# Performance work log

Measured on AMD Instinct MI355X. Metric: run time of the kernel, lower is better.

The kernel has to match this reference:

```python
import jax, jax.numpy as jnp
import numpy as np

B, S, HID, NH, CACHE = 2, 1024, 1024, 16, 4096
HD = HID // NH
HOT = max(4, CACHE // 4)
COLD = CACHE - HOT
COMP = HID // 2
EPS = 1e-5


def setup_inputs() -> dict:
    key = jax.random.key(0)
    ks = jax.random.split(key, 16)
    std = 0.02
    inp = {
        'inputs': jax.random.normal(ks[0], (B, S, HID), jnp.float32),
        'hot_keys': std * jax.random.normal(ks[1], (HOT, HID), jnp.float32),
        'hot_values': std * jax.random.normal(ks[2], (HOT, HID), jnp.float32),
        'hot_age': jnp.zeros((HOT,), jnp.float32),
        'hot_access': jnp.zeros((HOT,), jnp.float32),
        'cold_keys': std * jax.random.normal(ks[3], (COLD, HID), jnp.float32),
        'cold_values': std * jax.random.normal(ks[4], (COLD, HID), jnp.float32),
        'cold_age': jnp.zeros((COLD,), jnp.float32),
        'cold_access': jnp.zeros((COLD,), jnp.float32),
        # linear weights stored [in, out] (y = x @ W + b)
        'Wq': std * jax.random.normal(ks[5], (HID, HID), jnp.float32),
        'bq': jnp.zeros((HID,), jnp.float32),
        'Wk': std * jax.random.normal(ks[6], (HID, HID), jnp.float32),
        'bk': jnp.zeros((HID,), jnp.float32),
        'Wv': std * jax.random.normal(ks[7], (HID, HID), jnp.float32),
        'bv': jnp.zeros((HID,), jnp.float32),
        'Wo': std * jax.random.normal(ks[8], (HID, HID), jnp.float32),
        'bo': jnp.zeros((HID,), jnp.float32),
        'Wc': (1.0 / np.sqrt(HID)) * jax.random.normal(ks[9], (HID, COMP), jnp.float32),
        'bc': jnp.zeros((COMP,), jnp.float32),
        'Wd': (1.0 / np.sqrt(COMP)) * jax.random.normal(ks[10], (COMP, HID), jnp.float32),
        'bd': jnp.zeros((HID,), jnp.float32),
        'gamma': jnp.ones((HID,), jnp.float32),
        'beta': jnp.zeros((HID,), jnp.float32),
    }
    return inp


def _cache_level(q, cache_k, v_flat, age, access, Wk, bk, Wo, bo):
    # q: [B, NH, S, HD]; cache_k/v_flat: [C, HID]
    C = cache_k.shape[0]
    k = (cache_k @ Wk + bk).reshape(C, NH, HD)
    v = v_flat.reshape(C, NH, HD)
    scores = jnp.einsum('bhsd,chd->bhsc', q, k) / np.sqrt(HD)
    scores = scores + (-0.1 * age + 0.05 * access)  # broadcast over [B,H,S,C]
    attn = jax.nn.softmax(scores, axis=-1)
    out = jnp.einsum('bhsc,chd->bhsd', attn, v)
    out = out.transpose(0, 2, 1, 3).reshape(q.shape[0], q.shape[2], HID)
    return out @ Wo + bo


def reference(inputs, hot_keys, hot_values, hot_age, hot_access,
              cold_keys, cold_values, cold_age, cold_access,
              Wq, bq, Wk, bk, Wv, bv, Wo, bo, Wc, bc, Wd, bd, gamma, beta):
    q = (inputs @ Wq + bq).reshape(B, S, NH, HD).transpose(0, 2, 1, 3)
    # hot tier: values through value_net
    hot_v = hot_values @ Wv + bv
    hot_out = _cache_level(q, hot_keys, hot_v, hot_age, hot_access, Wk, bk, Wo, bo)
    # cold tier: values through compressor -> decompressor
    cold_v = (cold_values @ Wc + bc) @ Wd + bd
    cold_out = _cache_level(q, cold_keys, cold_v, cold_age, cold_access, Wk, bk, Wo, bo)
    x = hot_out + cold_out
    mu = jnp.mean(x, axis=-1, keepdims=True)
    var = jnp.mean(jnp.square(x - mu), axis=-1, keepdims=True)
    return (x - mu) / jnp.sqrt(var + EPS) * gamma + beta
```

## Files before the change

kernel.cpp:

```cpp
#include <hip/hip_runtime.h>

#define BBATCH 2
#define SS   1024
#define HID  1024
#define NH   16
#define HD   64
#define HOT  1024
#define COLD 3072
#define COMP 512

typedef __attribute__((ext_vector_type(8))) short s8v;
typedef __attribute__((ext_vector_type(4))) float f4v;
typedef unsigned short u16;
typedef unsigned int   u32;

__device__ __forceinline__ float b2f(u16 u){ return __uint_as_float(((u32)u)<<16); }
__device__ __forceinline__ u16 f2b(float f){
  u32 u = __float_as_uint(f);
  u += 0x7FFF + ((u>>16)&1);
  return (u16)(u>>16);
}
__device__ __forceinline__ u32 pk2r(u32 a, u32 b){
  return __builtin_amdgcn_perm(b + 0x8000u, a + 0x8000u, 0x07060302u);
}
__device__ __forceinline__ float ldsc(const void* p, int i, int isf32){
  return isf32 ? ((const float*)p)[i] : b2f(((const u16*)p)[i]);
}

__global__ void detect_kernel(const u32* __restrict__ gamma_raw, u32* __restrict__ flag){
  if (threadIdx.x == 0) flag[0] = (gamma_raw[0] == 0x3F800000u) ? 1u : 0u;
}

__global__ __launch_bounds__(256) void bias_kernel(
    const void* __restrict__ h_age, const void* __restrict__ h_acc,
    const void* __restrict__ c_age, const void* __restrict__ c_acc,
    float* __restrict__ BiasH, float* __restrict__ BiasC, const u32* __restrict__ flag)
{
  const int f = (int)flag[0];
  const int i = blockIdx.x * 256 + threadIdx.x;
  if (i < HOT) BiasH[i] = -0.1f * ldsc(h_age, i, f) + 0.05f * ldsc(h_acc, i, f);
  const int j = i - HOT;
  if (j >= 0 && j < COLD) BiasC[j] = -0.1f * ldsc(c_age, j, f) + 0.05f * ldsc(c_acc, j, f);
}

struct CDesc { const void* S; u16* D; int tile0, pad; };
struct CBatch { CDesc d[5]; int nd; };

__global__ __launch_bounds__(256) void convert_multi(CBatch cb, const u32* __restrict__ flag)
{
  int di = 0;
  for (int i = 1; i < cb.nd; i++) if ((int)blockIdx.x >= cb.d[i].tile0) di = i;
  const CDesc g = cb.d[di];
  const int f = (int)flag[0];
  const size_t e0 = (size_t)(blockIdx.x - g.tile0) * 2048 + (size_t)threadIdx.x * 8;
  if (f) {
    const float* s = (const float*)g.S + e0;
    const uint4 x = *(const uint4*)s, y = *(const uint4*)(s + 4);
    *(uint4*)(g.D + e0) =
      (uint4){ pk2r(x.x,x.y), pk2r(x.z,x.w), pk2r(y.x,y.y), pk2r(y.z,y.w) };
  } else {
    *(uint4*)(g.D + e0) = *(const uint4*)((const u16*)g.S + e0);
  }
}

struct TDesc { const void* S; u16* D; int R, C, cshift, tile0; };
struct TBatch { TDesc d[6]; int nd; };

__global__ __launch_bounds__(256) void transpose_kernel(TBatch tb, const u32* __restrict__ flag)
{
  __shared__ __align__(16) u16 Tt[64][72];
  int di = 0;
  for (int i = 1; i < tb.nd; i++) if ((int)blockIdx.x >= tb.d[i].tile0) di = i;
  const TDesc g = tb.d[di];
  const int local = blockIdx.x - g.tile0;
  const int ty = local >> g.cshift;
  const int tx = local & ((1 << g.cshift) - 1);
  const int r0 = ty * 64, c0 = tx * 64;
  const int f = (int)flag[0];
  const int t = threadIdx.x;
  const int sr = t >> 2, sc = (t & 3) * 16;

  union { uint4 q[2]; u16 h[16]; } u;
  if (f) {
    const float* s = (const float*)g.S + (size_t)(r0 + sr) * g.C + c0 + sc;
    const uint4 a = *(const uint4*)s,     b = *(const uint4*)(s + 4);
    const uint4 c = *(const uint4*)(s + 8), d2 = *(const uint4*)(s + 12);
    u.q[0] = (uint4){ pk2r(a.x,a.y), pk2r(a.z,a.w), pk2r(b.x,b.y), pk2r(b.z,b.w) };
    u.q[1] = (uint4){ pk2r(c.x,c.y), pk2r(c.z,c.w), pk2r(d2.x,d2.y), pk2r(d2.z,d2.w) };
  } else {
    const u16* s = (const u16*)g.S + (size_t)(r0 + sr) * g.C + c0 + sc;
    u.q[0] = *(const uint4*)s;  u.q[1] = *(const uint4*)(s + 8);
  }
  #pragma unroll
  for (int i = 0; i < 16; i++) Tt[sc + i][sr] = u.h[i];
  __syncthreads();

  const int dc = t >> 2, dr = (t & 3) * 16;
  const uint4 o0 = *(const uint4*)&Tt[dc][dr];
  const uint4 o1 = *(const uint4*)&Tt[dc][dr + 8];
  u16* dp = g.D + (size_t)(c0 + dc) * g.R + r0 + dr;
  *(uint4*)dp = o0;  *(uint4*)(dp + 8) = o1;
}

#define BM 128
#define BN 64
#define BK 32
struct GemmDesc {
  const void* A; const u16* BT; const void* bias; u16* C;
  int aflag, bcol0, M, N, K, nxlog, tile0, ctrans;
  float bias_scale;
};
struct GemmBatch { GemmDesc d[6]; int nd; };

__global__ __launch_bounds__(256) void gemm_multi(GemmBatch bat, const u32* __restrict__ flag)
{
  __shared__ __align__(16) u16 As[BM][BK + 8];
  __shared__ __align__(16) u16 Bs[BN][BK + 8];

  int di = 0;
  for (int i = 1; i < bat.nd; i++) if ((int)blockIdx.x >= bat.d[i].tile0) di = i;
  const GemmDesc g = bat.d[di];
  const int local = blockIdx.x - g.tile0;
  const int ty = local >> g.nxlog;
  const int tx = local - (ty << g.nxlog);
  const int m0 = ty * BM, n0 = tx * BN;

  const int f  = (int)flag[0];
  const int af = g.aflag ? f : 0;

  const int tid  = threadIdx.x;
  const int lane = tid & 63, wave = tid >> 6;
  const int quad = lane >> 4, l15 = lane & 15;
  const int wy = wave >> 1, wx = wave & 1;

  f4v acc[4][2];
  #pragma unroll
  for (int i = 0; i < 4; i++)
    #pragma unroll
    for (int j = 0; j < 2; j++) acc[i][j] = (f4v){0.f,0.f,0.f,0.f};

  const int ar = tid >> 1, ac = (tid & 1) * 16;
  const int br = tid >> 2, bc = (tid & 3) * 8;

  uint4 a0, a1, a2, a3;
  uint4 b0;

  auto load_tile = [&](int kk) {
    if (af) {
      const float* s = (const float*)g.A + (size_t)(m0 + ar) * g.K + kk + ac;
      a0 = *(const uint4*)s;       a1 = *(const uint4*)(s + 4);
      a2 = *(const uint4*)(s + 8); a3 = *(const uint4*)(s + 12);
    } else {
      const u16* s = (const u16*)g.A + (size_t)(m0 + ar) * g.K + kk + ac;
      a0 = *(const uint4*)s;  a1 = *(const uint4*)(s + 8);
    }
    const u16* bs = g.BT + (size_t)(g.bcol0 + n0 + br) * g.K + kk + bc;
    b0 = *(const uint4*)bs;
  };

  load_tile(0);

  for (int k0 = 0; k0 < g.K; k0 += BK) {
    __syncthreads();
    if (af) {
      *(uint4*)&As[ar][ac] =
        (uint4){ pk2r(a0.x,a0.y), pk2r(a0.z,a0.w), pk2r(a1.x,a1.y), pk2r(a1.z,a1.w) };
      *(uint4*)&As[ar][ac + 8] =
        (uint4){ pk2r(a2.x,a2.y), pk2r(a2.z,a2.w), pk2r(a3.x,a3.y), pk2r(a3.z,a3.w) };
    } else {
      *(uint4*)&As[ar][ac] = a0;  *(uint4*)&As[ar][ac + 8] = a1;
    }
    *(uint4*)&Bs[br][bc] = b0;
    __syncthreads();

    if (k0 + BK < g.K) load_tile(k0 + BK);

    s8v afr[4], bfr[2];
    #pragma unroll
    for (int i = 0; i < 4; i++)
      afr[i] = *(const s8v*)&As[wy * 64 + i * 16 + l15][quad * 8];
    #pragma unroll
    for (int j = 0; j < 2; j++)
      bfr[j] = *(const s8v*)&Bs[wx * 32 + j * 16 + l15][quad * 8];

    #pragma unroll
    for (int j = 0; j < 2; j++)
      #pragma unroll
      for (int i = 0; i < 4; i++)
        acc[i][j] = __builtin_amdgcn_mfma_f32_16x16x32_bf16(afr[i], bfr[j], acc[i][j], 0, 0, 0);
  }

  if (g.ctrans) {
    #pragma unroll
    for (int j = 0; j < 2; j++) {
      const int col = n0 + wx * 32 + j * 16 + l15;
      const float bv = ldsc(g.bias, g.bcol0 + col, f) * g.bias_scale;
      #pragma unroll
      for (int i = 0; i < 4; i++) {
        const int row = m0 + wy * 64 + i * 16 + quad * 4;
        u16 t4[4];
        #pragma unroll
        for (int r = 0; r < 4; r++) t4[r] = f2b(acc[i][j][r] + bv);
        *(uint2*)&g.C[(size_t)col * g.M + row] = *(uint2*)t4;
      }
    }
  } else {
    #pragma unroll
    for (int j = 0; j < 2; j++) {
      const int col = n0 + wx * 32 + j * 16 + l15;
      const float bv = ldsc(g.bias, g.bcol0 + col, f) * g.bias_scale;
      #pragma unroll
      for (int i = 0; i < 4; i++) {
        const int row = m0 + wy * 64 + i * 16 + quad * 4;
        #pragma unroll
        for (int r = 0; r < 4; r++)
          g.C[(size_t)(row + r) * g.N + col] = f2b(acc[i][j][r] + bv);
      }
    }
  }
}

#define KV(row, blk) (((row) << 6) + ((((blk) ^ ((row) & 7))) << 3))

__global__ __launch_bounds__(256, 4) void attn_kernel(
    const u16* __restrict__ Q,
    const u16* __restrict__ KHg, const u16* __restrict__ VHT,
    const u16* __restrict__ KCg, const u16* __restrict__ VCT,
    const float* __restrict__ BiasH, const float* __restrict__ BiasC,
    float* __restrict__ HotOut, float* __restrict__ ColdNum3, float* __restrict__ ColdZ3,
    int NG, int glog)
{
  __shared__ __align__(16) u16 Ks[64 * 64];
  __shared__ __align__(16) u16 Vs[64 * 64];

  const int tid  = threadIdx.x;
  const int lane = tid & 63, wave = tid >> 6;
  const int quad = lane >> 4, l15 = lane & 15;

  const int bx    = blockIdx.x;
  const int slice = bx & 3;
  const int sblk  = (bx >> 2) & 15;
  const int h     = (bx >> 6) & ((1 << glog) - 1);
  const int b     = bx >> (6 + glog);

  const int rowbase = b * SS + sblk * 64;
  const int hoff  = h * HD;
  const int myrow = wave * 16;

  const bool hot = (slice == 0);
  const u16*  Kt   = hot ? KHg : KCg;
  const u16*  Vt   = hot ? VHT : VCT;
  const float* Bias = hot ? BiasH : BiasC;
  const int   e0  = hot ? 0 : (slice - 1) * 1024;
  const int   ldv = hot ? HOT : COLD;

  const u16* qp = Q + (size_t)(rowbase + myrow + l15) * NG + hoff + quad * 8;
  const s8v aq0 = *(const s8v*)qp;
  const s8v aq1 = *(const s8v*)(qp + 32);

  const int rk = tid >> 2, cb2 = (tid & 3) * 2, sk = (tid & 3) * 16;
  const u16* kbase = Kt + (size_t)(e0 + rk) * NG + hoff + sk;
  const u16* vbase = Vt + (size_t)(hoff + rk) * ldv + e0 + sk;
  uint4 kr0 = *(const uint4*)kbase, kr1 = *(const uint4*)(kbase + 8);
  uint4 vr0 = *(const uint4*)vbase, vr1 = *(const uint4*)(vbase + 8);

  u16* kw0 = &Ks[KV(rk, cb2)];     u16* kw1 = &Ks[KV(rk, cb2 + 1)];
  u16* vw0 = &Vs[KV(rk, cb2)];     u16* vw1 = &Vs[KV(rk, cb2 + 1)];

  f4v o[4];
  #pragma unroll
  for (int j = 0; j < 4; j++) o[j] = (f4v){0.f,0.f,0.f,0.f};
  float zs = 0.f;

  for (int c0 = 0; c0 < 1024; c0 += 64) {
    __syncthreads();
    *(uint4*)kw0 = kr0;  *(uint4*)kw1 = kr1;
    *(uint4*)vw0 = vr0;  *(uint4*)vw1 = vr1;
    __syncthreads();
    if (c0 + 64 < 1024) {
      const u16* kn = kbase + (size_t)(c0 + 64) * NG;
      const u16* vn = vbase + (c0 + 64);
      kr0 = *(const uint4*)kn;  kr1 = *(const uint4*)(kn + 8);
      vr0 = *(const uint4*)vn;  vr1 = *(const uint4*)(vn + 8);
    }

    #pragma unroll
    for (int h2 = 0; h2 < 2; h2++) {
      const s8v ka0 = *(const s8v*)&Ks[KV(h2 * 32 + l15, quad)];
      const s8v ka1 = *(const s8v*)&Ks[KV(h2 * 32 + l15, 4 + quad)];
      const s8v kb0 = *(const s8v*)&Ks[KV(h2 * 32 + 16 + l15, quad)];
      const s8v kb1 = *(const s8v*)&Ks[KV(h2 * 32 + 16 + l15, 4 + quad)];
      f4v s0 = (f4v){0.f,0.f,0.f,0.f}, s1 = (f4v){0.f,0.f,0.f,0.f};
      s0 = __builtin_amdgcn_mfma_f32_16x16x32_bf16(ka0, aq0, s0, 0, 0, 0);
      s0 = __builtin_amdgcn_mfma_f32_16x16x32_bf16(ka1, aq1, s0, 0, 0, 0);
      s1 = __builtin_amdgcn_mfma_f32_16x16x32_bf16(kb0, aq0, s1, 0, 0, 0);
      s1 = __builtin_amdgcn_mfma_f32_16x16x32_bf16(kb1, aq1, s1, 0, 0, 0);

      const int cg0 = e0 + c0 + h2 * 32 + quad * 4;
      const float4 bi0 = *(const float4*)&Bias[cg0];
      const float4 bi1 = *(const float4*)&Bias[cg0 + 16];
      float p0[4], p1[4];
      p0[0] = __expf(fminf(s0[0] * 0.125f + bi0.x, 30.f));
      p0[1] = __expf(fminf(s0[1] * 0.125f + bi0.y, 30.f));
      p0[2] = __expf(fminf(s0[2] * 0.125f + bi0.z, 30.f));
      p0[3] = __expf(fminf(s0[3] * 0.125f + bi0.w, 30.f));
      p1[0] = __expf(fminf(s1[0] * 0.125f + bi1.x, 30.f));
      p1[1] = __expf(fminf(s1[1] * 0.125f + bi1.y, 30.f));
      p1[2] = __expf(fminf(s1[2] * 0.125f + bi1.z, 30.f));
      p1[3] = __expf(fminf(s1[3] * 0.125f + bi1.w, 30.f));
      zs += p0[0] + p0[1] + p0[2] + p0[3] + p1[0] + p1[1] + p1[2] + p1[3];

      const u32 W0 = pk2r(__float_as_uint(p0[0]), __float_as_uint(p0[1]));
      const u32 W1 = pk2r(__float_as_uint(p0[2]), __float_as_uint(p0[3]));
      const u32 W2 = pk2r(__float_as_uint(p1[0]), __float_as_uint(p1[1]));
      const u32 W3 = pk2r(__float_as_uint(p1[2]), __float_as_uint(p1[3]));

      union { u32 w[4]; s8v v; } ap;
      #pragma unroll
      for (int t = 0; t < 4; t++) {
        const int srcl = (((quad << 1) + (t >> 1)) & 3) * 16 + l15;
        const u32 lo = __shfl((t & 1) ? W1 : W0, srcl, 64);
        const u32 hi = __shfl((t & 1) ? W3 : W2, srcl, 64);
        ap.w[t] = (quad >= 2) ? hi : lo;
      }

      #pragma unroll
      for (int j2 = 0; j2 < 4; j2++) {
        const s8v bv = *(const s8v*)&Vs[KV(j2 * 16 + l15, h2 * 4 + quad)];
        o[j2] = __builtin_amdgcn_mfma_f32_16x16x32_bf16(ap.v, bv, o[j2], 0, 0, 0);
      }
    }
  }

  zs += __shfl_xor(zs, 16, 64);
  zs += __shfl_xor(zs, 32, 64);

  if (hot) {
    float rz[4];
    #pragma unroll
    for (int r = 0; r < 4; r++) rz[r] = 1.0f / __shfl(zs, quad * 4 + r, 64);
    #pragma unroll
    for (int j = 0; j < 4; j++) {
      const int col = hoff + j * 16 + l15;
      #pragma unroll
      for (int r = 0; r < 4; r++) {
        const int row = rowbase + myrow + quad * 4 + r;
        HotOut[(size_t)row * NG + col] = o[j][r] * rz[r];
      }
    }
  } else {
    float* CN = ColdNum3 + (size_t)(slice - 1) * 2048 * NG;
    #pragma unroll
    for (int j = 0; j < 4; j++) {
      const int col = hoff + j * 16 + l15;
      #pragma unroll
      for (int r = 0; r < 4; r++) {
        const int row = rowbase + myrow + quad * 4 + r;
        CN[(size_t)row * NG + col] = o[j][r];
      }
    }
    if (lane < 16)
      ColdZ3[((size_t)(slice - 1) * 2048 + rowbase + myrow + lane) * (1 << glog) + h] = zs;
  }
}

__global__ __launch_bounds__(256) void combine_kernel(
    const float* __restrict__ HotOut, const float* __restrict__ ColdNum3,
    const float* __restrict__ ColdZ3, u16* __restrict__ ATT,
    int att_ld, int att_c0, int NG, int glog)
{
  const int gid   = blockIdx.x * 256 + threadIdx.x;
  const int shift = 4 + glog;
  const int row   = gid >> shift;
  const int c4    = (gid & ((1 << shift) - 1)) << 2;
  const int h     = c4 >> 6;
  const int G     = 1 << glog;
  const size_t ps = (size_t)2048 * NG;
  const size_t zs = (size_t)2048 * G;

  const float4 hv = *(const float4*)&HotOut[(size_t)row * NG + c4];
  const float4 c1 = *(const float4*)&ColdNum3[(size_t)row * NG + c4];
  const float4 c2 = *(const float4*)&ColdNum3[ps + (size_t)row * NG + c4];
  const float4 c3 = *(const float4*)&ColdNum3[2 * ps + (size_t)row * NG + c4];
  const float z = ColdZ3[(size_t)row * G + h] + ColdZ3[zs + (size_t)row * G + h]
                + ColdZ3[2 * zs + (size_t)row * G + h];
  const float zi = 1.0f / z;

  u16 ov[4];
  ov[0] = f2b(hv.x + (c1.x + c2.x + c3.x) * zi);
  ov[1] = f2b(hv.y + (c1.y + c2.y + c3.y) * zi);
  ov[2] = f2b(hv.z + (c1.z + c2.z + c3.z) * zi);
  ov[3] = f2b(hv.w + (c1.w + c2.w + c3.w) * zi);
  *(uint2*)&ATT[(size_t)row * att_ld + att_c0 + c4] = *(uint2*)ov;
}

__global__ __launch_bounds__(256) void ln_kernel(
    const u16* __restrict__ X, const void* __restrict__ gamma,
    const void* __restrict__ beta, void* __restrict__ outp,
    const u32* __restrict__ flag)
{
  __shared__ float red[4];
  const int f = (int)flag[0];
  const int row = blockIdx.x, tid = threadIdx.x;
  const u16* xr = X + (size_t)row * HID;

  float x[4];
  { union { uint2 q; u16 hx[4]; } bx2;
    bx2.q = *(const uint2*)(xr + tid * 4);
    #pragma unroll
    for (int i = 0; i < 4; i++) x[i] = b2f(bx2.hx[i]); }

  float s = x[0] + x[1] + x[2] + x[3];
  #pragma unroll
  for (int m = 1; m < 64; m <<= 1) s += __shfl_xor(s, m, 64);
  if ((tid & 63) == 0) red[tid >> 6] = s;
  __syncthreads();
  const float mu = (red[0] + red[1] + red[2] + red[3]) * (1.0f / HID);
  __syncthreads();

  float v = 0.f;
  #pragma unroll
  for (int i = 0; i < 4; i++) { const float d = x[i] - mu; v += d * d; }
  #pragma unroll
  for (int m = 1; m < 64; m <<= 1) v += __shfl_xor(v, m, 64);
  if ((tid & 63) == 0) red[tid >> 6] = v;
  __syncthreads();
  const float var  = (red[0] + red[1] + red[2] + red[3]) * (1.0f / HID);
  const float rstd = 1.0f / sqrtf(var + 1e-5f);

  #pragma unroll
  for (int i = 0; i < 4; i++) {
    const int col = tid * 4 + i;
    const float val = (x[i] - mu) * rstd * ldsc(gamma, col, f) + ldsc(beta, col, f);
    if (f) ((float*)outp)[(size_t)row * HID + col] = val;
    else   ((u16*) outp)[(size_t)row * HID + col] = f2b(val);
  }
}

extern "C" void kernel_launch(void* const* d_in, const int* in_sizes, int n_in,
                              void* d_out, int out_size, void* d_ws, size_t ws_size,
                              hipStream_t stream)
{
  const void* inputs      = d_in[0];
  const void* hot_keys    = d_in[1];
  const void* hot_values  = d_in[2];
  const void* hot_age     = d_in[3];
  const void* hot_access  = d_in[4];
  const void* cold_keys   = d_in[5];
  const void* cold_values = d_in[6];
  const void* cold_age    = d_in[7];
  const void* cold_access = d_in[8];
  const void* Wq = d_in[9];   const void* bq = d_in[10];
  const void* Wk = d_in[11];  const void* bk = d_in[12];
  const void* Wv = d_in[13];  const void* bv = d_in[14];
  const void* Wo = d_in[15];  const void* bo = d_in[16];
  const void* Wc = d_in[17];  const void* bc = d_in[18];
  const void* Wd = d_in[19];  const void* bd = d_in[20];
  const void* gamma = d_in[21];
  const void* beta  = d_in[22];

  const size_t FIX    = 256 + 16384;
  const size_t WT     = (size_t)10 * 1024 * 1024;
  const size_t COPIES = (size_t)10240 * 1024 * 2;
  const size_t XB     = (size_t)2048 * HID * 2;
  auto PART = [](int Gc){ return (size_t)2048 * (64 * Gc) * 16 + (size_t)2048 * Gc * 12; };
  auto BUFS = [](int Gc){ return (size_t)10240 * (64 * Gc) * 2; };
  auto MX   = [](size_t a, size_t b){ return a > b ? a : b; };

  int G = 0, docopy = 0;
  { const size_t needF = FIX + WT + MX(COPIES, MX(PART(16), XB)) + BUFS(16);
    if (ws_size >= needF) { G = 16; docopy = 1; } }
  for (int c = 8; c >= 2 && !G; c >>= 1)
    if (ws_size >= FIX + WT + COPIES + MX(PART(c), XB) + BUFS(c)) { G = c; docopy = 1; }
  for (int c = 8; c >= 2 && !G; c >>= 1)
    if (ws_size >= FIX + WT + MX(PART(c), XB) + BUFS(c)) { G = c; docopy = 0; }
  if (!G) return;
  const int glog = (G == 16) ? 4 : (G == 8 ? 3 : (G == 4 ? 2 : 1));
  const int NG = 64 * G;
  const bool full = (G == 16);

  char* base  = (char*)d_ws;
  u32*  flag  = (u32*)base;
  float* BiasH = (float*)(base + 256);
  float* BiasC = BiasH + HOT;
  u16* WqT = (u16*)(base + FIX);
  u16* WkT = WqT + (size_t)1024 * 1024;
  u16* WvT = WkT + (size_t)1024 * 1024;
  u16* WoT = WvT + (size_t)1024 * 1024;
  u16* WcT = WoT + (size_t)1024 * 1024;
  u16* WdT = WcT + (size_t)512 * 1024;
  char* rp0 = base + FIX + WT;

  u16* inputsB = (u16*)rp0;
  u16* hotkB   = inputsB + (size_t)2048 * 1024;
  u16* coldkB  = hotkB   + (size_t)1024 * 1024;
  u16* hotvB   = coldkB  + (size_t)3072 * 1024;
  u16* coldvB  = hotvB   + (size_t)1024 * 1024;

  char* rp = rp0 + ((docopy && !full) ? COPIES : 0);
  u16*   X        = (u16*)rp;
  float* HotOut   = (float*)rp;
  float* ColdNum3 = (float*)(rp + (size_t)2048 * NG * 4);
  float* ColdZ3   = (float*)(rp + (size_t)2048 * NG * 16);
  const size_t Rbytes = full ? MX(COPIES, MX(PART(16), XB)) : MX(PART(G), XB);
  u16* Qg  = (u16*)(rp + Rbytes);
  u16* KHg = Qg  + (size_t)2048 * NG;
  u16* KCg = KHg + (size_t)HOT  * NG;
  u16* VHT = KCg + (size_t)COLD * NG;
  u16* VCT = VHT + (size_t)HOT  * NG;
  u16* ATT   = (u16*)d_out;
  u16* CVmid = (u16*)d_out + (size_t)2048 * 1024;

  const void* Aq = docopy ? (const void*)inputsB : inputs;
  const void* Ahk = docopy ? (const void*)hotkB  : hot_keys;
  const void* Ack = docopy ? (const void*)coldkB : cold_keys;
  const void* Ahv = docopy ? (const void*)hotvB  : hot_values;
  const void* Acv = docopy ? (const void*)coldvB : cold_values;
  const int afl = docopy ? 0 : 1;

  const dim3 blk(256);
  const int mQ = 2048 / BM, mH = HOT / BM, mC = COLD / BM;

  detect_kernel<<<dim3(1), dim3(64), 0, stream>>>((const u32*)gamma, flag);
  bias_kernel<<<dim3((HOT + COLD) / 256), blk, 0, stream>>>(
      hot_age, hot_access, cold_age, cold_access, BiasH, BiasC, flag);

  if (docopy) {
    CBatch cb; cb.nd = 5; int t = 0;
    cb.d[0] = { inputs,      inputsB, t, 0 }; t += 1024;
    cb.d[1] = { hot_keys,    hotkB,   t, 0 }; t += 512;
    cb.d[2] = { cold_keys,   coldkB,  t, 0 }; t += 1536;
    cb.d[3] = { hot_values,  hotvB,   t, 0 }; t += 512;
    cb.d[4] = { cold_values, coldvB,  t, 0 }; t += 1536;
    convert_multi<<<dim3(t), blk, 0, stream>>>(cb, flag);
  }
  { TBatch tb; tb.nd = 6; int t = 0;
    tb.d[0] = { Wq, WqT, 1024, 1024, 4, t }; t += 256;
    tb.d[1] = { Wk, WkT, 1024, 1024, 4, t }; t += 256;
    tb.d[2] = { Wv, WvT, 1024, 1024, 4, t }; t += 256;
    tb.d[3] = { Wo, WoT, 1024, 1024, 4, t }; t += 256;
    tb.d[4] = { Wc, WcT, 1024,  512, 3, t }; t += 128;
    tb.d[5] = { Wd, WdT,  512, 1024, 4, t }; t += 128;
    transpose_kernel<<<dim3(t), blk, 0, stream>>>(tb, flag);
  }

  if (full) {
    { GemmBatch bb; bb.nd = 5; int t = 0;
      bb.d[0] = { Aq,  WqT, bq, Qg,    afl, 0, 2048, 1024, 1024, 4, t, 0, 1.0f }; t += 16 * mQ;
      bb.d[1] = { Ahk, WkT, bk, KHg,   afl, 0, HOT,  1024, 1024, 4, t, 0, 1.0f }; t += 16 * mH;
      bb.d[2] = { Ack, WkT, bk, KCg,   afl, 0, COLD, 1024, 1024, 4, t, 0, 1.0f }; t += 16 * mC;
      bb.d[3] = { Ahv, WvT, bv, VHT,   afl, 0, HOT,  1024, 1024, 4, t, 1, 1.0f }; t += 16 * mH;
      bb.d[4] = { Acv, WcT, bc, CVmid, afl, 0, COLD,  512, 1024, 3, t, 0, 1.0f }; t += 8 * mC;
      gemm_multi<<<dim3(t), blk, 0, stream>>>(bb, flag);
    }
    { GemmBatch bb; bb.nd = 1;
      bb.d[0] = { CVmid, WdT, bd, VCT, 0, 0, COLD, 1024, 512, 4, 0, 1, 1.0f };
      gemm_multi<<<dim3(16 * mC), blk, 0, stream>>>(bb, flag);
    }
    attn_kernel<<<dim3(BBATCH * 16 * 16 * 4), blk, 0, stream>>>(
        Qg, KHg, VHT, KCg, VCT, BiasH, BiasC, HotOut, ColdNum3, ColdZ3, NG, glog);
    combine_kernel<<<dim3((2048 * (NG / 4)) / 256), blk, 0, stream>>>(
        HotOut, ColdNum3, ColdZ3, ATT, HID, 0, NG, glog);
  } else {
    { GemmBatch bb; bb.nd = 5; int t = 0;
      bb.d[0] = { Aq,  WqT, bq, Qg,    afl, 0, 2048, NG,  1024, glog, t, 0, 1.0f }; t += G * mQ;
      bb.d[1] = { Ahk, WkT, bk, KHg,   afl, 0, HOT,  NG,  1024, glog, t, 0, 1.0f }; t += G * mH;
      bb.d[2] = { Ack, WkT, bk, KCg,   afl, 0, COLD, NG,  1024, glog, t, 0, 1.0f }; t += G * mC;
      bb.d[3] = { Ahv, WvT, bv, VHT,   afl, 0, HOT,  NG,  1024, glog, t, 1, 1.0f }; t += G * mH;
      bb.d[4] = { Acv, WcT, bc, CVmid, afl, 0, COLD, 512, 1024, 3,    t, 0, 1.0f }; t += 8 * mC;
      gemm_multi<<<dim3(t), blk, 0, stream>>>(bb, flag);
    }
    { GemmBatch bb; bb.nd = 1;
      bb.d[0] = { CVmid, WdT, bd, VCT, 0, 0, COLD, NG, 512, glog, 0, 1, 1.0f };
      gemm_multi<<<dim3(G * mC), blk, 0, stream>>>(bb, flag);
    }
    attn_kernel<<<dim3(BBATCH * G * 16 * 4), blk, 0, stream>>>(
        Qg, KHg, VHT, KCg, VCT, BiasH, BiasC, HotOut, ColdNum3, ColdZ3, NG, glog);
    combine_kernel<<<dim3((2048 * (NG / 4)) / 256), blk, 0, stream>>>(
        HotOut, ColdNum3, ColdZ3, ATT, HID, 0, NG, glog);

    for (int p = 1; p < NH / G; ++p) {
      const int c0 = p * NG;
      GemmBatch bb; bb.nd = 5; int t = 0;
      bb.d[0] = { Aq,    WqT, bq, Qg,  afl, c0, 2048, NG, 1024, glog, t, 0, 1.0f }; t += G * mQ;
      bb.d[1] = { Ahk,   WkT, bk, KHg, afl, c0, HOT,  NG, 1024, glog, t, 0, 1.0f }; t += G * mH;
      bb.d[2] = { Ack,   WkT, bk, KCg, afl, c0, COLD, NG, 1024, glog, t, 0, 1.0f }; t += G * mC;
      bb.d[3] = { Ahv,   WvT, bv, VHT, afl, c0, HOT,  NG, 1024, glog, t, 1, 1.0f }; t += G * mH;
      bb.d[4] = { CVmid, WdT, bd, VCT, 0,   c0, COLD, NG, 512,  glog, t, 1, 1.0f }; t += G * mC;
      gemm_multi<<<dim3(t), blk, 0, stream>>>(bb, flag);

      attn_kernel<<<dim3(BBATCH * G * 16 * 4), blk, 0, stream>>>(
          Qg, KHg, VHT, KCg, VCT, BiasH, BiasC, HotOut, ColdNum3, ColdZ3, NG, glog);
      combine_kernel<<<dim3((2048 * (NG / 4)) / 256), blk, 0, stream>>>(
          HotOut, ColdNum3, ColdZ3, ATT, HID, c0, NG, glog);
    }
  }

  { GemmBatch bb; bb.nd = 1;
    bb.d[0] = { ATT, WoT, bo, X, 0, 0, 2048, 1024, 1024, 4, 0, 0, 2.0f };
    gemm_multi<<<dim3(16 * mQ), blk, 0, stream>>>(bb, flag);
  }
  ln_kernel<<<dim3(2048), blk, 0, stream>>>(X, gamma, beta, d_out, flag);
}
```

Before: 311.6 us.

## Process two 16-row query tiles per wave in attention kernel to reuse K/V tiles

Each wave in the attention kernel now handles 32 query rows instead of 16, so a block covers 128 rows and the grid is halved. Every K/V tile staged in shared memory is reused for twice as many query rows, cutting global loads, LDS traffic and barriers per unit of work. The cost is roughly doubled accumulator and register use per wave (the occupancy hint in launch bounds was dropped) and half as many blocks, which may lower occupancy and latency hiding.

```diff
diff --git a/kernel.cpp b/kernel.cpp
--- a/kernel.cpp
+++ b/kernel.cpp
@@ -222,7 +222,7 @@
 
 #define KV(row, blk) (((row) << 6) + ((((blk) ^ ((row) & 7))) << 3))
 
-__global__ __launch_bounds__(256, 4) void attn_kernel(
+__global__ __launch_bounds__(256) void attn_kernel(
     const u16* __restrict__ Q,
     const u16* __restrict__ KHg, const u16* __restrict__ VHT,
     const u16* __restrict__ KCg, const u16* __restrict__ VCT,
@@ -239,13 +239,13 @@
 
   const int bx    = blockIdx.x;
   const int slice = bx & 3;
-  const int sblk  = (bx >> 2) & 15;
-  const int h     = (bx >> 6) & ((1 << glog) - 1);
-  const int b     = bx >> (6 + glog);
-
-  const int rowbase = b * SS + sblk * 64;
+  const int sblk  = (bx >> 2) & 7;
+  const int h     = (bx >> 5) & ((1 << glog) - 1);
+  const int b     = bx >> (5 + glog);
+
+  const int rowbase = b * SS + sblk * 128;
   const int hoff  = h * HD;
-  const int myrow = wave * 16;
+  const int myrow = wave * 32;
 
   const bool hot = (slice == 0);
   const u16*  Kt   = hot ? KHg : KCg;
@@ -257,6 +257,9 @@
   const u16* qp = Q + (size_t)(rowbase + myrow + l15) * NG + hoff + quad * 8;
   const s8v aq0 = *(const s8v*)qp;
   const s8v aq1 = *(const s8v*)(qp + 32);
+  const u16* qp1 = qp + (size_t)16 * NG;
+  const s8v aq2 = *(const s8v*)qp1;
+  const s8v aq3 = *(const s8v*)(qp1 + 32);
 
   const int rk = tid >> 2, cb2 = (tid & 3) * 2, sk = (tid & 3) * 16;
   const u16* kbase = Kt + (size_t)(e0 + rk) * NG + hoff + sk;
@@ -267,10 +270,10 @@
   u16* kw0 = &Ks[KV(rk, cb2)];     u16* kw1 = &Ks[KV(rk, cb2 + 1)];
   u16* vw0 = &Vs[KV(rk, cb2)];     u16* vw1 = &Vs[KV(rk, cb2 + 1)];
 
-  f4v o[4];
+  f4v o0[4], o1[4];
   #pragma unroll
-  for (int j = 0; j < 4; j++) o[j] = (f4v){0.f,0.f,0.f,0.f};
-  float zs = 0.f;
+  for (int j = 0; j < 4; j++) { o0[j] = (f4v){0.f,0.f,0.f,0.f}; o1[j] = (f4v){0.f,0.f,0.f,0.f}; }
+  float zs0 = 0.f, zs1 = 0.f;
 
   for (int c0 = 0; c0 < 1024; c0 += 64) {
     __syncthreads();
@@ -290,62 +293,95 @@
       const s8v ka1 = *(const s8v*)&Ks[KV(h2 * 32 + l15, 4 + quad)];
       const s8v kb0 = *(const s8v*)&Ks[KV(h2 * 32 + 16 + l15, quad)];
       const s8v kb1 = *(const s8v*)&Ks[KV(h2 * 32 + 16 + l15, 4 + quad)];
-      f4v s0 = (f4v){0.f,0.f,0.f,0.f}, s1 = (f4v){0.f,0.f,0.f,0.f};
-      s0 = __builtin_amdgcn_mfma_f32_16x16x32_bf16(ka0, aq0, s0, 0, 0, 0);
-      s0 = __builtin_amdgcn_mfma_f32_16x16x32_bf16(ka1, aq1, s0, 0, 0, 0);
-      s1 = __builtin_amdgcn_mfma_f32_16x16x32_bf16(kb0, aq0, s1, 0, 0, 0);
-      s1 = __builtin_amdgcn_mfma_f32_16x16x32_bf16(kb1, aq1, s1, 0, 0, 0);
 
       const int cg0 = e0 + c0 + h2 * 32 + quad * 4;
       const float4 bi0 = *(const float4*)&Bias[cg0];
       const float4 bi1 = *(const float4*)&Bias[cg0 + 16];
-      float p0[4], p1[4];
-      p0[0] = __expf(fminf(s0[0] * 0.125f + bi0.x, 30.f));
-      p0[1] = __expf(fminf(s0[1] * 0.125f + bi0.y, 30.f));
-      p0[2] = __expf(fminf(s0[2] * 0.125f + bi0.z, 30.f));
-      p0[3] = __expf(fminf(s0[3] * 0.125f + bi0.w, 30.f));
-      p1[0] = __expf(fminf(s1[0] * 0.125f + bi1.x, 30.f));
-      p1[1] = __expf(fminf(s1[1] * 0.125f + bi1.y, 30.f));
-      p1[2] = __expf(fminf(s1[2] * 0.125f + bi1.z, 30.f));
-      p1[3] = __expf(fminf(s1[3] * 0.125f + bi1.w, 30.f));
-      zs += p0[0] + p0[1] + p0[2] + p0[3] + p1[0] + p1[1] + p1[2] + p1[3];
-
-      const u32 W0 = pk2r(__float_as_uint(p0[0]), __float_as_uint(p0[1]));
-      const u32 W1 = pk2r(__float_as_uint(p0[2]), __float_as_uint(p0[3]));
-      const u32 W2 = pk2r(__float_as_uint(p1[0]), __float_as_uint(p1[1]));
-      const u32 W3 = pk2r(__float_as_uint(p1[2]), __float_as_uint(p1[3]));
-
-      union { u32 w[4]; s8v v; } ap;
-      #pragma unroll
-      for (int t = 0; t < 4; t++) {
-        const int srcl = (((quad << 1) + (t >> 1)) & 3) * 16 + l15;
-        const u32 lo = __shfl((t & 1) ? W1 : W0, srcl, 64);
-        const u32 hi = __shfl((t & 1) ? W3 : W2, srcl, 64);
-        ap.w[t] = (quad >= 2) ? hi : lo;
+
+      union { u32 w[4]; s8v v; } ap0, ap1;
+      {
+        f4v s0 = (f4v){0.f,0.f,0.f,0.f}, s1 = (f4v){0.f,0.f,0.f,0.f};
+        s0 = __builtin_amdgcn_mfma_f32_16x16x32_bf16(ka0, aq0, s0, 0, 0, 0);
+        s0 = __builtin_amdgcn_mfma_f32_16x16x32_bf16(ka1, aq1, s0, 0, 0, 0);
+        s1 = __builtin_amdgcn_mfma_f32_16x16x32_bf16(kb0, aq0, s1, 0, 0, 0);
+        s1 = __builtin_amdgcn_mfma_f32_16x16x32_bf16(kb1, aq1, s1, 0, 0, 0);
+        float p0[4], p1[4];
+        p0[0] = __expf(fminf(s0[0] * 0.125f + bi0.x, 30.f));
+        p0[1] = __expf(fminf(s0[1] * 0.125f + bi0.y, 30.f));
+        p0[2] = __expf(fminf(s0[2] * 0.125f + bi0.z, 30.f));
+        p0[3] = __expf(fminf(s0[3] * 0.125f + bi0.w, 30.f));
+        p1[0] = __expf(fminf(s1[0] * 0.125f + bi1.x, 30.f));
+        p1[1] = __expf(fminf(s1[1] * 0.125f + bi1.y, 30.f));
+        p1[2] = __expf(fminf(s1[2] * 0.125f + bi1.z, 30.f));
+        p1[3] = __expf(fminf(s1[3] * 0.125f + bi1.w, 30.f));
+        zs0 += p0[0] + p0[1] + p0[2] + p0[3] + p1[0] + p1[1] + p1[2] + p1[3];
+        const u32 W0 = pk2r(__float_as_uint(p0[0]), __float_as_uint(p0[1]));
+        const u32 W1 = pk2r(__float_as_uint(p0[2]), __float_as_uint(p0[3]));
+        const u32 W2 = pk2r(__float_as_uint(p1[0]), __float_as_uint(p1[1]));
+        const u32 W3 = pk2r(__float_as_uint(p1[2]), __float_as_uint(p1[3]));
+        #pragma unroll
+        for (int t = 0; t < 4; t++) {
+          const int srcl = (((quad << 1) + (t >> 1)) & 3) * 16 + l15;
+          const u32 lo = __shfl((t & 1) ? W1 : W0, srcl, 64);
+          const u32 hi = __shfl((t & 1) ? W3 : W2, srcl, 64);
+          ap0.w[t] = (quad >= 2) ? hi : lo;
+        }
       }
-
+      {
+        f4v s0 = (f4v){0.f,0.f,0.f,0.f}, s1 = (f4v){0.f,0.f,0.f,0.f};
+        s0 = __builtin_amdgcn_mfma_f32_16x16x32_bf16(ka0, aq2, s0, 0, 0, 0);
+        s0 = __builtin_amdgcn_mfma_f32_16x16x32_bf16(ka1, aq3, s0, 0, 0, 0);
+        s1 = __builtin_amdgcn_mfma_f32_16x16x32_bf16(kb0, aq2, s1, 0, 0, 0);
+        s1 = __builtin_amdgcn_mfma_f32_16x16x32_bf16(kb1, aq3, s1, 0, 0, 0);
+        float p0[4], p1[4];
+        p0[0] = __expf(fminf(s0[0] * 0.125f + bi0.x, 30.f));
+        p0[1] = __expf(fminf(s0[1] * 0.125f + bi0.y, 30.f));
+        p0[2] = __expf(fminf(s0[2] * 0.125f + bi0.z, 30.f));
+        p0[3] = __expf(fminf(s0[3] * 0.125f + bi0.w, 30.f));
+        p1[0] = __expf(fminf(s1[0] * 0.125f + bi1.x, 30.f));
+        p1[1] = __expf(fminf(s1[1] * 0.125f + bi1.y, 30.f));
+        p1[2] = __expf(fminf(s1[2] * 0.125f + bi1.z, 30.f));
+        p1[3] = __expf(fminf(s1[3] * 0.125f + bi1.w, 30.f));
+        zs1 += p0[0] + p0[1] + p0[2] + p0[3] + p1[0] + p1[1] + p1[2] + p1[3];
+        const u32 W0 = pk2r(__float_as_uint(p0[0]), __float_as_uint(p0[1]));
+        const u32 W1 = pk2r(__float_as_uint(p0[2]), __float_as_uint(p0[3]));
+        const u32 W2 = pk2r(__float_as_uint(p1[0]), __float_as_uint(p1[1]));
+        const u32 W3 = pk2r(__float_as_uint(p1[2]), __float_as_uint(p1[3]));
+        #pragma unroll
+        for (int t = 0; t < 4; t++) {
+          const int srcl = (((quad << 1) + (t >> 1)) & 3) * 16 + l15;
+          const u32 lo = __shfl((t & 1) ? W1 : W0, srcl, 64);
+          const u32 hi = __shfl((t & 1) ? W3 : W2, srcl, 64);
+          ap1.w[t] = (quad >= 2) ? hi : lo;
+        }
+      }
       #pragma unroll
       for (int j2 = 0; j2 < 4; j2++) {
         const s8v bv = *(const s8v*)&Vs[KV(j2 * 16 + l15, h2 * 4 + quad)];
-        o[j2] = __builtin_amdgcn_mfma_f32_16x16x32_bf16(ap.v, bv, o[j2], 0, 0, 0);
+        o0[j2] = __builtin_amdgcn_mfma_f32_16x16x32_bf16(ap0.v, bv, o0[j2], 0, 0, 0);
+        o1[j2] = __builtin_amdgcn_mfma_f32_16x16x32_bf16(ap1.v, bv, o1[j2], 0, 0, 0);
       }
     }
   }
 
-  zs += __shfl_xor(zs, 16, 64);
-  zs += __shfl_xor(zs, 32, 64);
+  zs0 += __shfl_xor(zs0, 16, 64);  zs0 += __shfl_xor(zs0, 32, 64);
+  zs1 += __shfl_xor(zs1, 16, 64);  zs1 += __shfl_xor(zs1, 32, 64);
 
   if (hot) {
-    float rz[4];
-    #pragma unroll
-    for (int r = 0; r < 4; r++) rz[r] = 1.0f / __shfl(zs, quad * 4 + r, 64);
+    float rz0[4], rz1[4];
+    #pragma unroll
+    for (int r = 0; r < 4; r++) {
+      rz0[r] = 1.0f / __shfl(zs0, quad * 4 + r, 64);
+      rz1[r] = 1.0f / __shfl(zs1, quad * 4 + r, 64);
+    }
     #pragma unroll
     for (int j = 0; j < 4; j++) {
       const int col = hoff + j * 16 + l15;
       #pragma unroll
       for (int r = 0; r < 4; r++) {
         const int row = rowbase + myrow + quad * 4 + r;
-        HotOut[(size_t)row * NG + col] = o[j][r] * rz[r];
+        HotOut[(size_t)row * NG + col]        = o0[j][r] * rz0[r];
+        HotOut[(size_t)(row + 16) * NG + col] = o1[j][r] * rz1[r];
       }
     }
   } else {
@@ -356,11 +392,15 @@
       #pragma unroll
       for (int r = 0; r < 4; r++) {
         const int row = rowbase + myrow + quad * 4 + r;
-        CN[(size_t)row * NG + col] = o[j][r];
+        CN[(size_t)row * NG + col]        = o0[j][r];
+        CN[(size_t)(row + 16) * NG + col] = o1[j][r];
       }
     }
-    if (lane < 16)
-      ColdZ3[((size_t)(slice - 1) * 2048 + rowbase + myrow + lane) * (1 << glog) + h] = zs;
+    if (lane < 16) {
+      const size_t zb = (size_t)(slice - 1) * 2048 + rowbase + myrow;
+      ColdZ3[(zb + lane) * (1 << glog) + h]      = zs0;
+      ColdZ3[(zb + 16 + lane) * (1 << glog) + h] = zs1;
+    }
   }
 }
 
@@ -557,7 +597,7 @@
       bb.d[0] = { CVmid, WdT, bd, VCT, 0, 0, COLD, 1024, 512, 4, 0, 1, 1.0f };
       gemm_multi<<<dim3(16 * mC), blk, 0, stream>>>(bb, flag);
     }
-    attn_kernel<<<dim3(BBATCH * 16 * 16 * 4), blk, 0, stream>>>(
+    attn_kernel<<<dim3(BBATCH * 16 * 8 * 4), blk, 0, stream>>>(
         Qg, KHg, VHT, KCg, VCT, BiasH, BiasC, HotOut, ColdNum3, ColdZ3, NG, glog);
     combine_kernel<<<dim3((2048 * (NG / 4)) / 256), blk, 0, stream>>>(
         HotOut, ColdNum3, ColdZ3, ATT, HID, 0, NG, glog);
@@ -574,7 +614,7 @@
       bb.d[0] = { CVmid, WdT, bd, VCT, 0, 0, COLD, NG, 512, glog, 0, 1, 1.0f };
       gemm_multi<<<dim3(G * mC), blk, 0, stream>>>(bb, flag);
     }
-    attn_kernel<<<dim3(BBATCH * G * 16 * 4), blk, 0, stream>>>(
+    attn_kernel<<<dim3(BBATCH * G * 8 * 4), blk, 0, stream>>>(
         Qg, KHg, VHT, KCg, VCT, BiasH, BiasC, HotOut, ColdNum3, ColdZ3, NG, glog);
     combine_kernel<<<dim3((2048 * (NG / 4)) / 256), blk, 0, stream>>>(
         HotOut, ColdNum3, ColdZ3, ATT, HID, 0, NG, glog);
@@ -589,7 +629,7 @@
       bb.d[4] = { CVmid, WdT, bd, VCT, 0,   c0, COLD, NG, 512,  glog, t, 1, 1.0f }; t += G * mC;
       gemm_multi<<<dim3(t), blk, 0, stream>>>(bb, flag);
 
-      attn_kernel<<<dim3(BBATCH * G * 16 * 4), blk, 0, stream>>>(
+      attn_kernel<<<dim3(BBATCH * G * 8 * 4), blk, 0, stream>>>(
           Qg, KHg, VHT, KCg, VCT, BiasH, BiasC, HotOut, ColdNum3, ColdZ3, NG, glog);
       combine_kernel<<<dim3((2048 * (NG / 4)) / 256), blk, 0, stream>>>(
           HotOut, ColdNum3, ColdZ3, ATT, HID, c0, NG, glog);
```

New measurement: 311.1 us. No clear change (-0.2%).
